# Kernel tuning notes

Hardware: AMD Instinct MI355X
Metric: run time of the kernel (lower is better)

The kernel has to match this reference:

```python
import jax, jax.numpy as jnp
import numpy as np

EPS = 1e-5

def _layernorm(h):
    # parameter-free LayerNorm over last dim (elementwise_affine=False)
    mu = jnp.mean(h, axis=-1, keepdims=True)
    var = jnp.mean(jnp.square(h - mu), axis=-1, keepdims=True)
    return (h - mu) / jnp.sqrt(var + EPS)

def setup_inputs() -> dict:
    key = jax.random.key(0)
    k1, k2, k3, k4 = jax.random.split(key, 4)
    B, D, F_, I = 16, 37, 4096, 64
    x = jax.random.normal(k1, (B, D, F_), dtype=jnp.float32)
    s = 1.0 / np.sqrt(D)  # ~ torch Linear default init scale
    Wq = jax.random.normal(k2, (D, I), dtype=jnp.float32) * s
    Wk = jax.random.normal(k3, (D, I), dtype=jnp.float32) * s
    Wv = jax.random.normal(k4, (D, I), dtype=jnp.float32) * s
    return {"x": x, "Wq": Wq, "Wk": Wk, "Wv": Wv}

def reference(x, Wq, Wk, Wv):
    # x: [B, depth, featuresize] -> entities [B, F, depth]
    xb = jnp.transpose(x, (0, 2, 1))
    q = _layernorm(jnp.einsum('bfd,di->bfi', xb, Wq))
    k = _layernorm(jnp.einsum('bfd,di->bfi', xb, Wk))
    v = _layernorm(jnp.einsum('bfd,di->bfi', xb, Wv))
    d = q.shape[-1]
    att = jnp.einsum('bqi,bki->bqk', q, k) / jnp.sqrt(jnp.float32(d))
    # faithful to torch: softmax over dim=1 (the query axis), not the key axis
    weights = jax.nn.softmax(att, axis=-2)
    return jnp.einsum('bqk,bki->bqi', weights, v)
```

## Files before the change

### kernel.cpp

```cpp
#include <hip/hip_runtime.h>
#include <math.h>

#define B_  16
#define D_  37
#define F_  4096
#define I_  64
#define EPS 1e-5f
#define QSCALE 0.18033688011112042f
#define NQS 2

typedef unsigned short u16;
typedef __bf16 bf16x8 __attribute__((ext_vector_type(8)));
typedef __bf16 bf16x2v __attribute__((ext_vector_type(2)));
typedef float  f32x16 __attribute__((ext_vector_type(16)));
typedef float  f32x2v __attribute__((ext_vector_type(2)));
typedef unsigned int u32x4 __attribute__((ext_vector_type(4)));
typedef int i32x2 __attribute__((ext_vector_type(2)));

#define ZERO16 {0,0,0,0, 0,0,0,0, 0,0,0,0, 0,0,0,0}
#define MFMA32(a, b, c) __builtin_amdgcn_mfma_f32_32x32x16_bf16((a), (b), (c), 0, 0, 0)

#if __has_builtin(__builtin_amdgcn_exp2f)
#define EX2(x) __builtin_amdgcn_exp2f(x)
#else
#define EX2(x) exp2f(x)
#endif
#if __has_builtin(__builtin_amdgcn_rcpf)
#define RCP(x) __builtin_amdgcn_rcpf(x)
#else
#define RCP(x) (1.f / (x))
#endif

__device__ __forceinline__ u16 f2b(float f) {
  unsigned u = __builtin_bit_cast(unsigned, f);
  return (u16)((u + 0x7fffu + ((u >> 16) & 1u)) >> 16);
}
__device__ __forceinline__ float b2f(u16 h) {
  return __builtin_bit_cast(float, (unsigned)h << 16);
}
__device__ __forceinline__ unsigned pk2(float lo, float hi) {
  f32x2v f = {lo, hi};
  bf16x2v h = __builtin_convertvector(f, bf16x2v);
  return __builtin_bit_cast(unsigned, h);
}

__device__ __forceinline__ void plswap(unsigned& a, unsigned& b) {
#if __has_builtin(__builtin_amdgcn_permlane32_swap)
  i32x2 r = __builtin_amdgcn_permlane32_swap((int)a, (int)b, false, false);
  a = (unsigned)r[0];
  b = (unsigned)r[1];
#else
  const int lh = (int)((threadIdx.x & 63) >> 5);
  unsigned pa = (unsigned)__shfl_xor((int)a, 32, 64);
  unsigned pb = (unsigned)__shfl_xor((int)b, 32, 64);
  unsigned na = lh ? pb : a;
  unsigned nb = lh ? b : pa;
  a = na;
  b = nb;
#endif
}

__device__ __forceinline__ void build_af(const f32x16& s, bf16x8& f0, bf16x8& f1) {
  float e[16];
#pragma unroll
  for (int r = 0; r < 16; ++r) e[r] = EX2(s[r]);
  unsigned a = pk2(e[0], e[1]),   bq = pk2(e[2], e[3]);
  unsigned c = pk2(e[4], e[5]),   d  = pk2(e[6], e[7]);
  plswap(a, c);
  plswap(bq, d);
  u32x4 v0 = {a, bq, c, d};
  f0 = __builtin_bit_cast(bf16x8, v0);
  unsigned ee = pk2(e[8], e[9]),  ff = pk2(e[10], e[11]);
  unsigned g  = pk2(e[12], e[13]), h = pk2(e[14], e[15]);
  plswap(ee, g);
  plswap(ff, h);
  u32x4 v1 = {ee, ff, g, h};
  f1 = __builtin_bit_cast(bf16x8, v1);
}

__device__ __forceinline__ bf16x8 ldfrag(const u16* base, int row, int kb) {
  return *(const bf16x8*)(base + (row << 6) + ((kb ^ (row & 7)) << 3));
}
__device__ __forceinline__ void stage16(u16* dst, const u16* src, int c, int spitch) {
  const int r = c >> 3, cb = c & 7;
  const int4 v = *(const int4*)(src + (size_t)r * spitch + (cb << 3));
  *(int4*)(dst + (r << 6) + ((cb ^ (r & 7)) << 3)) = v;
}
__device__ __forceinline__ int soff_l(int c) {
  const int r = c >> 3, cb = c & 7;
  return (r << 6) + ((cb ^ (r & 7)) << 3);
}
__device__ __forceinline__ int soff_g(int c, int spitch) {
  return (c >> 3) * spitch + ((c & 7) << 3);
}

__device__ __forceinline__ int swz512(int wg) {
  return (wg & 7) * 64 + (wg >> 3);
}

__global__ __launch_bounds__(256) void qkv_ln_k(
    const float* __restrict__ x,
    const float* __restrict__ Wq, const float* __restrict__ Wk,
    const float* __restrict__ Wv,
    u16* __restrict__ qn, u16* __restrict__ kn, u16* __restrict__ vt) {
  __shared__ float sW[3 * D_ * I_];
  __shared__ float xs[D_ * 64];
  __shared__ __align__(16) u16 vtile[64 * 72];

  const int t = threadIdx.x;
  const int b = blockIdx.y;
  const int f0 = blockIdx.x * 64;

  for (int i = t; i < D_ * I_; i += 256) {
    sW[i]               = Wq[i];
    sW[D_ * I_ + i]     = Wk[i];
    sW[2 * D_ * I_ + i] = Wv[i];
  }
  const float* xb = x + (size_t)b * D_ * F_ + f0;
  for (int i = t; i < D_ * 64; i += 256)
    xs[i] = xb[(size_t)(i >> 6) * F_ + (i & 63)];
  __syncthreads();

  const int lane = t & 63, w = t >> 6;

  for (int it = 0; it < 16; ++it) {
    const int fl = w * 16 + it;
    float hq = 0.f, hk = 0.f, hv = 0.f;
#pragma unroll
    for (int d = 0; d < D_; ++d) {
      const float xv = xs[d * 64 + fl];
      hq = fmaf(xv, sW[d * 64 + lane], hq);
      hk = fmaf(xv, sW[D_ * I_ + d * 64 + lane], hk);
      hv = fmaf(xv, sW[2 * D_ * I_ + d * 64 + lane], hv);
    }
    auto lnorm = [&](float a) -> float {
      float s = a;
#pragma unroll
      for (int o = 32; o > 0; o >>= 1) s += __shfl_xor(s, o, 64);
      const float mu = s * (1.f / 64.f);
      const float d0 = a - mu;
      float v = d0 * d0;
#pragma unroll
      for (int o = 32; o > 0; o >>= 1) v += __shfl_xor(v, o, 64);
      return d0 * rsqrtf(v * (1.f / 64.f) + EPS);
    };
    const size_t fo = ((size_t)b * F_ + f0 + fl) * I_ + lane;
    qn[fo] = f2b(lnorm(hq) * QSCALE);
    kn[fo] = f2b(lnorm(hk));
    vtile[lane * 72 + fl] = f2b(lnorm(hv));
  }
  __syncthreads();
  for (int p = 0; p < 2; ++p) {
    const int c = p * 256 + t;
    const int r = c >> 3, off = (c & 7) * 8;
    const int4 v = *(const int4*)&vtile[r * 72 + off];
    *(int4*)(vt + ((size_t)b * I_ + r) * F_ + f0 + off) = v;
  }
}

__global__ __launch_bounds__(256, 2) void attn_stats_k(
    const u16* __restrict__ qn, const u16* __restrict__ kn,
    float* __restrict__ zp) {
  __shared__ __align__(16) u16 sm[16384];

  const int t = threadIdx.x, lane = t & 63, w = t >> 6;
  const int l31 = lane & 31, lh = lane >> 5;
  const int lg = swz512((int)blockIdx.x);
  const int k0 = (lg & 15) * 256, b = (lg >> 4) & 15, qh = lg >> 8;

  const u16* kb = kn + ((size_t)b * F_ + k0) * I_;
#pragma unroll
  for (int p = 0; p < 8; ++p) stage16(sm, kb, p * 256 + t, 64);
  __syncthreads();
  bf16x8 kf[2][4];
#pragma unroll
  for (int kb2 = 0; kb2 < 2; ++kb2)
#pragma unroll
    for (int ic = 0; ic < 4; ++ic)
      kf[kb2][ic] = ldfrag(sm + (w * 64 + kb2 * 32) * 64, l31, ic * 2 + lh);
  __syncthreads();

  int qoff_l[2], qoff_g[2];
#pragma unroll
  for (int p = 0; p < 2; ++p) {
    const int c = p * 256 + t;
    qoff_l[p] = soff_l(c);
    qoff_g[p] = soff_g(c, 64);
  }

  const u16* qsrc = qn + ((size_t)b * F_ + qh * (F_ / NQS)) * I_;
#pragma unroll
  for (int p = 0; p < 2; ++p)
    *(int4*)(sm + qoff_l[p]) = *(const int4*)(qsrc + qoff_g[p]);
  qsrc += 64 * I_;

  float Zc[2][2] = {{0.f, 0.f}, {0.f, 0.f}};
  const int NC = F_ / NQS / 64;

  for (int c = 0; c < NC; ++c) {
    const int cur = (c & 1) * 4096;
    int4 qr0, qr1;
    const bool pf = (c + 1 < NC);
    if (pf) {
      qr0 = *(const int4*)(qsrc + qoff_g[0]);
      qr1 = *(const int4*)(qsrc + qoff_g[1]);
      qsrc += 64 * I_;
    }
    __syncthreads();

    f32x16 a00 = ZERO16, a01 = ZERO16, a10 = ZERO16, a11 = ZERO16;
    __builtin_amdgcn_s_setprio(1);
#pragma unroll
    for (int ic = 0; ic < 4; ++ic) {
      const bf16x8 q0f = ldfrag(sm + cur, l31, ic * 2 + lh);
      const bf16x8 q1f = ldfrag(sm + cur + 32 * 64, l31, ic * 2 + lh);
      a00 = MFMA32(q0f, kf[0][ic], a00);
      a01 = MFMA32(q0f, kf[1][ic], a01);
      a10 = MFMA32(q1f, kf[0][ic], a10);
      a11 = MFMA32(q1f, kf[1][ic], a11);
    }
    __builtin_amdgcn_s_setprio(0);
#pragma unroll
    for (int r = 0; r < 16; ++r) {
      Zc[0][0] += EX2(a00[r]);
      Zc[0][1] += EX2(a01[r]);
      Zc[1][0] += EX2(a10[r]);
      Zc[1][1] += EX2(a11[r]);
    }

    if (pf) {
      const int nxt = cur ^ 4096;
      *(int4*)(sm + nxt + qoff_l[0]) = qr0;
      *(int4*)(sm + nxt + qoff_l[1]) = qr1;
    }
  }

#pragma unroll
  for (int kb2 = 0; kb2 < 2; ++kb2) {
    float Zt = Zc[0][kb2] + Zc[1][kb2];
    Zt += __shfl_xor(Zt, 32, 64);
    if (lane < 32)
      zp[((size_t)qh * B_ + b) * F_ + k0 + w * 64 + kb2 * 32 + lane] = Zt;
  }
}

__global__ __launch_bounds__(256) void vscale_k(u16* __restrict__ vt,
                                                const float* __restrict__ zp) {
  const int b = blockIdx.y;
  const int off = (blockIdx.x * 256 + (int)threadIdx.x) * 8;
  const int k = off & (F_ - 1);
  const size_t BF = (size_t)B_ * F_;
  u16* p = vt + (size_t)b * I_ * F_ + off;
  const float* z = zp + (size_t)b * F_ + k;
  int4 raw = *(const int4*)p;
  u16 es[8], os[8];
  *(int4*)es = raw;
#pragma unroll
  for (int j = 0; j < 8; ++j) {
    const float v = b2f(es[j]);
    float zs = 0.f;
#pragma unroll
    for (int qh = 0; qh < NQS; ++qh) zs += z[qh * BF + j];
    os[j] = f2b(v * RCP(zs));
  }
  *(int4*)p = *(int4*)os;
}

__global__ __launch_bounds__(256, 2) void attn_out_k(
    const u16* __restrict__ qn, const u16* __restrict__ kn,
    const u16* __restrict__ vt, float* __restrict__ out,
    u16* __restrict__ pout) {
  __shared__ __align__(16) u16 sm[16384];

  const int t = threadIdx.x, lane = t & 63, w = t >> 6;
  const int l31 = lane & 31, lh = lane >> 5;
  const int lg = swz512((int)blockIdx.x);
  const int q0 = (lg & 15) * 256, b = (lg >> 4) & 15, ks = lg >> 8;

  const u16* qb = qn + ((size_t)b * F_ + q0) * I_;
#pragma unroll
  for (int p = 0; p < 8; ++p) stage16(sm, qb, p * 256 + t, 64);
  __syncthreads();
  bf16x8 qf[2][4];
#pragma unroll
  for (int qb2 = 0; qb2 < 2; ++qb2)
#pragma unroll
    for (int ic = 0; ic < 4; ++ic)
      qf[qb2][ic] = ldfrag(sm + (w * 64 + qb2 * 32) * 64, l31, ic * 2 + lh);
  __syncthreads();

  int off_l[2], kg[2], vg[2];
#pragma unroll
  for (int p = 0; p < 2; ++p) {
    const int c = p * 256 + t;
    off_l[p] = soff_l(c);
    kg[p] = soff_g(c, 64);
    vg[p] = soff_g(c, F_);
  }

  const u16* ksrc = kn + ((size_t)b * F_ + ks * (F_ / 2)) * I_;
  const u16* vsrc = vt + (size_t)b * I_ * F_ + ks * (F_ / 2);
#pragma unroll
  for (int p = 0; p < 2; ++p) {
    *(int4*)(sm + off_l[p])        = *(const int4*)(ksrc + kg[p]);
    *(int4*)(sm + 8192 + off_l[p]) = *(const int4*)(vsrc + vg[p]);
  }
  ksrc += 64 * I_;
  vsrc += 64;

  f32x16 o00 = ZERO16, o01 = ZERO16, o10 = ZERO16, o11 = ZERO16;
  const int NC = F_ / 2 / 64;

  for (int c = 0; c < NC; ++c) {
    const int cur = (c & 1) * 4096;
    int4 kr0, kr1, vr0, vr1;
    const bool pf = (c + 1 < NC);
    if (pf) {
      kr0 = *(const int4*)(ksrc + kg[0]);
      kr1 = *(const int4*)(ksrc + kg[1]);
      vr0 = *(const int4*)(vsrc + vg[0]);
      vr1 = *(const int4*)(vsrc + vg[1]);
      ksrc += 64 * I_;
      vsrc += 64;
    }
    __syncthreads();

    const u16* Kc = sm + cur;
    f32x16 s00 = ZERO16, s01 = ZERO16, s10 = ZERO16, s11 = ZERO16;
    __builtin_amdgcn_s_setprio(1);
#pragma unroll
    for (int ic = 0; ic < 4; ++ic) {
      const bf16x8 ak0 = ldfrag(Kc, l31, ic * 2 + lh);
      const bf16x8 ak1 = ldfrag(Kc + 32 * 64, l31, ic * 2 + lh);
      s00 = MFMA32(ak0, qf[0][ic], s00);
      s01 = MFMA32(ak0, qf[1][ic], s01);
      s10 = MFMA32(ak1, qf[0][ic], s10);
      s11 = MFMA32(ak1, qf[1][ic], s11);
    }
    __builtin_amdgcn_s_setprio(0);

    bf16x8 af[2][4];
    build_af(s00, af[0][0], af[0][1]);
    build_af(s10, af[0][2], af[0][3]);
    build_af(s01, af[1][0], af[1][1]);
    build_af(s11, af[1][2], af[1][3]);

    const u16* Vc = sm + 8192 + cur;
    __builtin_amdgcn_s_setprio(1);
#pragma unroll
    for (int kb4 = 0; kb4 < 4; ++kb4) {
      const bf16x8 bv0 = ldfrag(Vc, l31, kb4 * 2 + lh);
      const bf16x8 bv1 = ldfrag(Vc + 32 * 64, l31, kb4 * 2 + lh);
      o00 = MFMA32(af[0][kb4], bv0, o00);
      o01 = MFMA32(af[0][kb4], bv1, o01);
      o10 = MFMA32(af[1][kb4], bv0, o10);
      o11 = MFMA32(af[1][kb4], bv1, o11);
    }
    __builtin_amdgcn_s_setprio(0);

    if (pf) {
      const int nxt = cur ^ 4096;
      *(int4*)(sm + nxt + off_l[0])        = kr0;
      *(int4*)(sm + nxt + off_l[1])        = kr1;
      *(int4*)(sm + 8192 + nxt + off_l[0]) = vr0;
      *(int4*)(sm + 8192 + nxt + off_l[1]) = vr1;
    }
  }

  if (ks == 0) {
    float* ob = out + ((size_t)b * F_ + q0 + w * 64) * I_;
#pragma unroll
    for (int r = 0; r < 16; ++r) {
      const int qr = (r & 3) + 8 * (r >> 2) + 4 * lh;
      ob[(size_t)qr * I_ + l31]              = o00[r];
      ob[(size_t)qr * I_ + 32 + l31]         = o01[r];
      ob[(size_t)(32 + qr) * I_ + l31]       = o10[r];
      ob[(size_t)(32 + qr) * I_ + 32 + l31]  = o11[r];
    }
  } else {
    u16* pb = pout + ((size_t)b * F_ + q0 + w * 64) * I_;
#pragma unroll
    for (int r = 0; r < 16; ++r) {
      const int qr = (r & 3) + 8 * (r >> 2) + 4 * lh;
      pb[(size_t)qr * I_ + l31]              = f2b(o00[r]);
      pb[(size_t)qr * I_ + 32 + l31]         = f2b(o01[r]);
      pb[(size_t)(32 + qr) * I_ + l31]       = f2b(o10[r]);
      pb[(size_t)(32 + qr) * I_ + 32 + l31]  = f2b(o11[r]);
    }
  }
}

__global__ __launch_bounds__(256) void reduce_k(float* __restrict__ out,
                                                const u16* __restrict__ pout) {
  const size_t i = ((size_t)blockIdx.x * 256 + threadIdx.x) * 8;
  float4 a0 = *(const float4*)(out + i);
  float4 a1 = *(const float4*)(out + i + 4);
  int4 praw = *(const int4*)(pout + i);
  u16 es[8];
  *(int4*)es = praw;
  a0.x += b2f(es[0]); a0.y += b2f(es[1]); a0.z += b2f(es[2]); a0.w += b2f(es[3]);
  a1.x += b2f(es[4]); a1.y += b2f(es[5]); a1.z += b2f(es[6]); a1.w += b2f(es[7]);
  *(float4*)(out + i)     = a0;
  *(float4*)(out + i + 4) = a1;
}

extern "C" void kernel_launch(void* const* d_in, const int* in_sizes, int n_in,
                              void* d_out, int out_size, void* d_ws,
                              size_t ws_size, hipStream_t stream) {
  const float* x  = (const float*)d_in[0];
  const float* Wq = (const float*)d_in[1];
  const float* Wk = (const float*)d_in[2];
  const float* Wv = (const float*)d_in[3];
  float* out = (float*)d_out;

  const size_t NBF = (size_t)B_ * F_ * I_;
  u16* qn   = (u16*)d_ws;
  u16* kn   = qn + NBF;
  u16* vt   = kn + NBF;
  float* zp = (float*)(vt + NBF);
  u16* pout = (u16*)(zp + (size_t)NQS * B_ * F_);

  qkv_ln_k<<<dim3(F_ / 64, B_), 256, 0, stream>>>(x, Wq, Wk, Wv, qn, kn, vt);
  attn_stats_k<<<dim3(512), 256, 0, stream>>>(qn, kn, zp);
  vscale_k<<<dim3(I_ * F_ / 2048, B_), 256, 0, stream>>>(vt, zp);
  attn_out_k<<<dim3(512), 256, 0, stream>>>(qn, kn, vt, out, pout);
  reduce_k<<<dim3((int)(NBF / 2048)), 256, 0, stream>>>(out, pout);
}
```

Baseline: 234.6 us.

## Split attention into four query/key slices with fp32 partials and half-tile scoring

Doubles the grid of both attention kernels by splitting the stats pass into four query slices and the output pass into four key slices. Partial outputs are now written as fp32 instead of bf16, and reduce_k sums three partial planes. The inner loop computes scores one 32-row key half at a time to cut live registers, and launch bounds rise to three blocks per SM. This buys more parallelism and occupancy at the cost of more partial-output traffic and a heavier reduction.

Result: slower. 314.2 us (+33.9%).

```diff
diff --git a/kernel.cpp b/kernel.cpp
--- a/kernel.cpp
+++ b/kernel.cpp
@@ -7,7 +7,8 @@
 #define I_  64
 #define EPS 1e-5f
 #define QSCALE 0.18033688011112042f
-#define NQS 2
+#define NQS 4
+#define NKS 4
 
 typedef unsigned short u16;
 typedef __bf16 bf16x8 __attribute__((ext_vector_type(8)));
@@ -94,8 +95,8 @@
   return (c >> 3) * spitch + ((c & 7) << 3);
 }
 
-__device__ __forceinline__ int swz512(int wg) {
-  return (wg & 7) * 64 + (wg >> 3);
+__device__ __forceinline__ int swz1024(int wg) {
+  return (wg & 7) * 128 + (wg >> 3);
 }
 
 __global__ __launch_bounds__(256) void qkv_ln_k(
@@ -158,14 +159,14 @@
   }
 }
 
-__global__ __launch_bounds__(256, 2) void attn_stats_k(
+__global__ __launch_bounds__(256, 3) void attn_stats_k(
     const u16* __restrict__ qn, const u16* __restrict__ kn,
     float* __restrict__ zp) {
   __shared__ __align__(16) u16 sm[16384];
 
   const int t = threadIdx.x, lane = t & 63, w = t >> 6;
   const int l31 = lane & 31, lh = lane >> 5;
-  const int lg = swz512((int)blockIdx.x);
+  const int lg = swz1024((int)blockIdx.x);
   const int k0 = (lg & 15) * 256, b = (lg >> 4) & 15, qh = lg >> 8;
 
   const u16* kb = kn + ((size_t)b * F_ + k0) * I_;
@@ -266,15 +267,15 @@
   *(int4*)p = *(int4*)os;
 }
 
-__global__ __launch_bounds__(256, 2) void attn_out_k(
+__global__ __launch_bounds__(256, 3) void attn_out_k(
     const u16* __restrict__ qn, const u16* __restrict__ kn,
     const u16* __restrict__ vt, float* __restrict__ out,
-    u16* __restrict__ pout) {
+    float* __restrict__ pp) {
   __shared__ __align__(16) u16 sm[16384];
 
   const int t = threadIdx.x, lane = t & 63, w = t >> 6;
   const int l31 = lane & 31, lh = lane >> 5;
-  const int lg = swz512((int)blockIdx.x);
+  const int lg = swz1024((int)blockIdx.x);
   const int q0 = (lg & 15) * 256, b = (lg >> 4) & 15, ks = lg >> 8;
 
   const u16* qb = qn + ((size_t)b * F_ + q0) * I_;
@@ -298,8 +299,8 @@
     vg[p] = soff_g(c, F_);
   }
 
-  const u16* ksrc = kn + ((size_t)b * F_ + ks * (F_ / 2)) * I_;
-  const u16* vsrc = vt + (size_t)b * I_ * F_ + ks * (F_ / 2);
+  const u16* ksrc = kn + ((size_t)b * F_ + ks * (F_ / NKS)) * I_;
+  const u16* vsrc = vt + (size_t)b * I_ * F_ + ks * (F_ / NKS);
 #pragma unroll
   for (int p = 0; p < 2; ++p) {
     *(int4*)(sm + off_l[p])        = *(const int4*)(ksrc + kg[p]);
@@ -309,7 +310,7 @@
   vsrc += 64;
 
   f32x16 o00 = ZERO16, o01 = ZERO16, o10 = ZERO16, o11 = ZERO16;
-  const int NC = F_ / 2 / 64;
+  const int NC = F_ / NKS / 64;
 
   for (int c = 0; c < NC; ++c) {
     const int cur = (c & 1) * 4096;
@@ -326,37 +327,59 @@
     __syncthreads();
 
     const u16* Kc = sm + cur;
-    f32x16 s00 = ZERO16, s01 = ZERO16, s10 = ZERO16, s11 = ZERO16;
-    __builtin_amdgcn_s_setprio(1);
-#pragma unroll
-    for (int ic = 0; ic < 4; ++ic) {
-      const bf16x8 ak0 = ldfrag(Kc, l31, ic * 2 + lh);
-      const bf16x8 ak1 = ldfrag(Kc + 32 * 64, l31, ic * 2 + lh);
-      s00 = MFMA32(ak0, qf[0][ic], s00);
-      s01 = MFMA32(ak0, qf[1][ic], s01);
-      s10 = MFMA32(ak1, qf[0][ic], s10);
-      s11 = MFMA32(ak1, qf[1][ic], s11);
-    }
-    __builtin_amdgcn_s_setprio(0);
-
-    bf16x8 af[2][4];
-    build_af(s00, af[0][0], af[0][1]);
-    build_af(s10, af[0][2], af[0][3]);
-    build_af(s01, af[1][0], af[1][1]);
-    build_af(s11, af[1][2], af[1][3]);
-
     const u16* Vc = sm + 8192 + cur;
-    __builtin_amdgcn_s_setprio(1);
-#pragma unroll
-    for (int kb4 = 0; kb4 < 4; ++kb4) {
-      const bf16x8 bv0 = ldfrag(Vc, l31, kb4 * 2 + lh);
-      const bf16x8 bv1 = ldfrag(Vc + 32 * 64, l31, kb4 * 2 + lh);
-      o00 = MFMA32(af[0][kb4], bv0, o00);
-      o01 = MFMA32(af[0][kb4], bv1, o01);
-      o10 = MFMA32(af[1][kb4], bv0, o10);
-      o11 = MFMA32(af[1][kb4], bv1, o11);
-    }
-    __builtin_amdgcn_s_setprio(0);
+
+    {
+      f32x16 s0 = ZERO16, s1 = ZERO16;
+      __builtin_amdgcn_s_setprio(1);
+#pragma unroll
+      for (int ic = 0; ic < 4; ++ic) {
+        const bf16x8 ak = ldfrag(Kc, l31, ic * 2 + lh);
+        s0 = MFMA32(ak, qf[0][ic], s0);
+        s1 = MFMA32(ak, qf[1][ic], s1);
+      }
+      __builtin_amdgcn_s_setprio(0);
+      bf16x8 af[2][2];
+      build_af(s0, af[0][0], af[0][1]);
+      build_af(s1, af[1][0], af[1][1]);
+      __builtin_amdgcn_s_setprio(1);
+#pragma unroll
+      for (int kb4 = 0; kb4 < 2; ++kb4) {
+        const bf16x8 bv0 = ldfrag(Vc, l31, kb4 * 2 + lh);
+        const bf16x8 bv1 = ldfrag(Vc + 32 * 64, l31, kb4 * 2 + lh);
+        o00 = MFMA32(af[0][kb4], bv0, o00);
+        o01 = MFMA32(af[0][kb4], bv1, o01);
+        o10 = MFMA32(af[1][kb4], bv0, o10);
+        o11 = MFMA32(af[1][kb4], bv1, o11);
+      }
+      __builtin_amdgcn_s_setprio(0);
+    }
+
+    {
+      f32x16 s0 = ZERO16, s1 = ZERO16;
+      __builtin_amdgcn_s_setprio(1);
+#pragma unroll
+      for (int ic = 0; ic < 4; ++ic) {
+        const bf16x8 ak = ldfrag(Kc + 32 * 64, l31, ic * 2 + lh);
+        s0 = MFMA32(ak, qf[0][ic], s0);
+        s1 = MFMA32(ak, qf[1][ic], s1);
+      }
+      __builtin_amdgcn_s_setprio(0);
+      bf16x8 af[2][2];
+      build_af(s0, af[0][0], af[0][1]);
+      build_af(s1, af[1][0], af[1][1]);
+      __builtin_amdgcn_s_setprio(1);
+#pragma unroll
+      for (int kb4 = 2; kb4 < 4; ++kb4) {
+        const bf16x8 bv0 = ldfrag(Vc, l31, kb4 * 2 + lh);
+        const bf16x8 bv1 = ldfrag(Vc + 32 * 64, l31, kb4 * 2 + lh);
+        o00 = MFMA32(af[0][kb4 - 2], bv0, o00);
+        o01 = MFMA32(af[0][kb4 - 2], bv1, o01);
+        o10 = MFMA32(af[1][kb4 - 2], bv0, o10);
+        o11 = MFMA32(af[1][kb4 - 2], bv1, o11);
+      }
+      __builtin_amdgcn_s_setprio(0);
+    }
 
     if (pf) {
       const int nxt = cur ^ 4096;
@@ -367,39 +390,33 @@
     }
   }
 
-  if (ks == 0) {
-    float* ob = out + ((size_t)b * F_ + q0 + w * 64) * I_;
-#pragma unroll
-    for (int r = 0; r < 16; ++r) {
-      const int qr = (r & 3) + 8 * (r >> 2) + 4 * lh;
-      ob[(size_t)qr * I_ + l31]              = o00[r];
-      ob[(size_t)qr * I_ + 32 + l31]         = o01[r];
-      ob[(size_t)(32 + qr) * I_ + l31]       = o10[r];
-      ob[(size_t)(32 + qr) * I_ + 32 + l31]  = o11[r];
-    }
-  } else {
-    u16* pb = pout + ((size_t)b * F_ + q0 + w * 64) * I_;
-#pragma unroll
-    for (int r = 0; r < 16; ++r) {
-      const int qr = (r & 3) + 8 * (r >> 2) + 4 * lh;
-      pb[(size_t)qr * I_ + l31]              = f2b(o00[r]);
-      pb[(size_t)qr * I_ + 32 + l31]         = f2b(o01[r]);
-      pb[(size_t)(32 + qr) * I_ + l31]       = f2b(o10[r]);
-      pb[(size_t)(32 + qr) * I_ + 32 + l31]  = f2b(o11[r]);
-    }
+  float* ob = (ks == 0 ? out
+                       : pp + (size_t)(ks - 1) * ((size_t)B_ * F_ * I_)) +
+              ((size_t)b * F_ + q0 + w * 64) * I_;
+#pragma unroll
+  for (int r = 0; r < 16; ++r) {
+    const int qr = (r & 3) + 8 * (r >> 2) + 4 * lh;
+    ob[(size_t)qr * I_ + l31]              = o00[r];
+    ob[(size_t)qr * I_ + 32 + l31]         = o01[r];
+    ob[(size_t)(32 + qr) * I_ + l31]       = o10[r];
+    ob[(size_t)(32 + qr) * I_ + 32 + l31]  = o11[r];
   }
 }
 
 __global__ __launch_bounds__(256) void reduce_k(float* __restrict__ out,
-                                                const u16* __restrict__ pout) {
+                                                const float* __restrict__ pp) {
+  const size_t NBF = (size_t)B_ * F_ * I_;
   const size_t i = ((size_t)blockIdx.x * 256 + threadIdx.x) * 8;
   float4 a0 = *(const float4*)(out + i);
   float4 a1 = *(const float4*)(out + i + 4);
-  int4 praw = *(const int4*)(pout + i);
-  u16 es[8];
-  *(int4*)es = praw;
-  a0.x += b2f(es[0]); a0.y += b2f(es[1]); a0.z += b2f(es[2]); a0.w += b2f(es[3]);
-  a1.x += b2f(es[4]); a1.y += b2f(es[5]); a1.z += b2f(es[6]); a1.w += b2f(es[7]);
+#pragma unroll
+  for (int pl = 0; pl < NKS - 1; ++pl) {
+    const float* q = pp + (size_t)pl * NBF + i;
+    const float4 b0 = *(const float4*)q;
+    const float4 b1 = *(const float4*)(q + 4);
+    a0.x += b0.x; a0.y += b0.y; a0.z += b0.z; a0.w += b0.w;
+    a1.x += b1.x; a1.y += b1.y; a1.z += b1.z; a1.w += b1.w;
+  }
   *(float4*)(out + i)     = a0;
   *(float4*)(out + i + 4) = a1;
 }
@@ -418,11 +435,11 @@
   u16* kn   = qn + NBF;
   u16* vt   = kn + NBF;
   float* zp = (float*)(vt + NBF);
-  u16* pout = (u16*)(zp + (size_t)NQS * B_ * F_);
+  float* pp = zp + (size_t)NQS * B_ * F_;
 
   qkv_ln_k<<<dim3(F_ / 64, B_), 256, 0, stream>>>(x, Wq, Wk, Wv, qn, kn, vt);
-  attn_stats_k<<<dim3(512), 256, 0, stream>>>(qn, kn, zp);
+  attn_stats_k<<<dim3(1024), 256, 0, stream>>>(qn, kn, zp);
   vscale_k<<<dim3(I_ * F_ / 2048, B_), 256, 0, stream>>>(vt, zp);
-  attn_out_k<<<dim3(512), 256, 0, stream>>>(qn, kn, vt, out, pout);
-  reduce_k<<<dim3((int)(NBF / 2048)), 256, 0, stream>>>(out, pout);
-}
+  attn_out_k<<<dim3(1024), 256, 0, stream>>>(qn, kn, vt, out, pp);
+  reduce_k<<<dim3((int)(NBF / 2048)), 256, 0, stream>>>(out, pp);
+}
```

## Stage two 64-row tiles per barrier and load resident fragments directly from global

Applied to the files above, without the earlier changes.

Both attention kernels now double-buffer 128-row chunks split into two 64-row halves. Each loop iteration needs only one __syncthreads, and the global loads for the second half are issued between the two half computations. The resident K (stats kernel) and Q (output kernel) MFMA fragments are read straight from global memory into registers instead of being staged through shared memory, which drops two barriers and an LDS round trip. The output kernel's shared memory doubles to 64 KB, which may limit occupancy under the two-blocks-per-CU launch bound.

Result: no change. 232.9 us (-0.7%).

```diff
diff --git a/kernel.cpp b/kernel.cpp
--- a/kernel.cpp
+++ b/kernel.cpp
@@ -8,6 +8,7 @@
 #define EPS 1e-5f
 #define QSCALE 0.18033688011112042f
 #define NQS 2
+#define NKS 2
 
 typedef unsigned short u16;
 typedef __bf16 bf16x8 __attribute__((ext_vector_type(8)));
@@ -81,11 +82,6 @@
 __device__ __forceinline__ bf16x8 ldfrag(const u16* base, int row, int kb) {
   return *(const bf16x8*)(base + (row << 6) + ((kb ^ (row & 7)) << 3));
 }
-__device__ __forceinline__ void stage16(u16* dst, const u16* src, int c, int spitch) {
-  const int r = c >> 3, cb = c & 7;
-  const int4 v = *(const int4*)(src + (size_t)r * spitch + (cb << 3));
-  *(int4*)(dst + (r << 6) + ((cb ^ (r & 7)) << 3)) = v;
-}
 __device__ __forceinline__ int soff_l(int c) {
   const int r = c >> 3, cb = c & 7;
   return (r << 6) + ((cb ^ (r & 7)) << 3);
@@ -168,17 +164,13 @@
   const int lg = swz512((int)blockIdx.x);
   const int k0 = (lg & 15) * 256, b = (lg >> 4) & 15, qh = lg >> 8;
 
-  const u16* kb = kn + ((size_t)b * F_ + k0) * I_;
-#pragma unroll
-  for (int p = 0; p < 8; ++p) stage16(sm, kb, p * 256 + t, 64);
-  __syncthreads();
+  const u16* kp = kn + ((size_t)b * F_ + k0 + w * 64 + l31) * I_ + lh * 8;
   bf16x8 kf[2][4];
 #pragma unroll
   for (int kb2 = 0; kb2 < 2; ++kb2)
 #pragma unroll
     for (int ic = 0; ic < 4; ++ic)
-      kf[kb2][ic] = ldfrag(sm + (w * 64 + kb2 * 32) * 64, l31, ic * 2 + lh);
-  __syncthreads();
+      kf[kb2][ic] = *(const bf16x8*)(kp + kb2 * 32 * I_ + ic * 16);
 
   int qoff_l[2], qoff_g[2];
 #pragma unroll
@@ -190,30 +182,22 @@
 
   const u16* qsrc = qn + ((size_t)b * F_ + qh * (F_ / NQS)) * I_;
 #pragma unroll
-  for (int p = 0; p < 2; ++p)
-    *(int4*)(sm + qoff_l[p]) = *(const int4*)(qsrc + qoff_g[p]);
-  qsrc += 64 * I_;
+  for (int s = 0; s < 2; ++s)
+#pragma unroll
+    for (int p = 0; p < 2; ++p)
+      *(int4*)(sm + s * 4096 + qoff_l[p]) =
+          *(const int4*)(qsrc + s * 64 * I_ + qoff_g[p]);
+  qsrc += 128 * I_;
 
   float Zc[2][2] = {{0.f, 0.f}, {0.f, 0.f}};
-  const int NC = F_ / NQS / 64;
-
-  for (int c = 0; c < NC; ++c) {
-    const int cur = (c & 1) * 4096;
-    int4 qr0, qr1;
-    const bool pf = (c + 1 < NC);
-    if (pf) {
-      qr0 = *(const int4*)(qsrc + qoff_g[0]);
-      qr1 = *(const int4*)(qsrc + qoff_g[1]);
-      qsrc += 64 * I_;
-    }
-    __syncthreads();
-
+
+  auto qcompute = [&](const u16* Qc) {
     f32x16 a00 = ZERO16, a01 = ZERO16, a10 = ZERO16, a11 = ZERO16;
     __builtin_amdgcn_s_setprio(1);
 #pragma unroll
     for (int ic = 0; ic < 4; ++ic) {
-      const bf16x8 q0f = ldfrag(sm + cur, l31, ic * 2 + lh);
-      const bf16x8 q1f = ldfrag(sm + cur + 32 * 64, l31, ic * 2 + lh);
+      const bf16x8 q0f = ldfrag(Qc, l31, ic * 2 + lh);
+      const bf16x8 q1f = ldfrag(Qc + 32 * 64, l31, ic * 2 + lh);
       a00 = MFMA32(q0f, kf[0][ic], a00);
       a01 = MFMA32(q0f, kf[1][ic], a01);
       a10 = MFMA32(q1f, kf[0][ic], a10);
@@ -227,11 +211,32 @@
       Zc[1][0] += EX2(a10[r]);
       Zc[1][1] += EX2(a11[r]);
     }
-
-    if (pf) {
-      const int nxt = cur ^ 4096;
+  };
+
+  const int NC = F_ / NQS / 128;
+
+  for (int c = 0; c < NC; ++c) {
+    const int cur = (c & 1) * 8192;
+    const int nxt = cur ^ 8192;
+    const bool pf = (c + 1 < NC);
+    __syncthreads();
+    int4 qr0, qr1;
+    if (pf) {
+      qr0 = *(const int4*)(qsrc + qoff_g[0]);
+      qr1 = *(const int4*)(qsrc + qoff_g[1]);
+    }
+    qcompute(sm + cur);
+    if (pf) {
       *(int4*)(sm + nxt + qoff_l[0]) = qr0;
       *(int4*)(sm + nxt + qoff_l[1]) = qr1;
+      qr0 = *(const int4*)(qsrc + 64 * I_ + qoff_g[0]);
+      qr1 = *(const int4*)(qsrc + 64 * I_ + qoff_g[1]);
+    }
+    qcompute(sm + cur + 4096);
+    if (pf) {
+      *(int4*)(sm + nxt + 4096 + qoff_l[0]) = qr0;
+      *(int4*)(sm + nxt + 4096 + qoff_l[1]) = qr1;
+      qsrc += 128 * I_;
     }
   }
 
@@ -270,24 +275,20 @@
     const u16* __restrict__ qn, const u16* __restrict__ kn,
     const u16* __restrict__ vt, float* __restrict__ out,
     u16* __restrict__ pout) {
-  __shared__ __align__(16) u16 sm[16384];
+  __shared__ __align__(16) u16 sm[32768];
 
   const int t = threadIdx.x, lane = t & 63, w = t >> 6;
   const int l31 = lane & 31, lh = lane >> 5;
   const int lg = swz512((int)blockIdx.x);
   const int q0 = (lg & 15) * 256, b = (lg >> 4) & 15, ks = lg >> 8;
 
-  const u16* qb = qn + ((size_t)b * F_ + q0) * I_;
-#pragma unroll
-  for (int p = 0; p < 8; ++p) stage16(sm, qb, p * 256 + t, 64);
-  __syncthreads();
+  const u16* qp = qn + ((size_t)b * F_ + q0 + w * 64 + l31) * I_ + lh * 8;
   bf16x8 qf[2][4];
 #pragma unroll
   for (int qb2 = 0; qb2 < 2; ++qb2)
 #pragma unroll
     for (int ic = 0; ic < 4; ++ic)
-      qf[qb2][ic] = ldfrag(sm + (w * 64 + qb2 * 32) * 64, l31, ic * 2 + lh);
-  __syncthreads();
+      qf[qb2][ic] = *(const bf16x8*)(qp + qb2 * 32 * I_ + ic * 16);
 
   int off_l[2], kg[2], vg[2];
 #pragma unroll
@@ -298,34 +299,23 @@
     vg[p] = soff_g(c, F_);
   }
 
-  const u16* ksrc = kn + ((size_t)b * F_ + ks * (F_ / 2)) * I_;
-  const u16* vsrc = vt + (size_t)b * I_ * F_ + ks * (F_ / 2);
-#pragma unroll
-  for (int p = 0; p < 2; ++p) {
-    *(int4*)(sm + off_l[p])        = *(const int4*)(ksrc + kg[p]);
-    *(int4*)(sm + 8192 + off_l[p]) = *(const int4*)(vsrc + vg[p]);
-  }
-  ksrc += 64 * I_;
-  vsrc += 64;
+  const u16* ksrc = kn + ((size_t)b * F_ + ks * (F_ / NKS)) * I_;
+  const u16* vsrc = vt + (size_t)b * I_ * F_ + ks * (F_ / NKS);
+#pragma unroll
+  for (int s = 0; s < 2; ++s)
+#pragma unroll
+    for (int p = 0; p < 2; ++p) {
+      *(int4*)(sm + s * 4096 + off_l[p]) =
+          *(const int4*)(ksrc + s * 64 * I_ + kg[p]);
+      *(int4*)(sm + 16384 + s * 4096 + off_l[p]) =
+          *(const int4*)(vsrc + s * 64 + vg[p]);
+    }
+  ksrc += 128 * I_;
+  vsrc += 128;
 
   f32x16 o00 = ZERO16, o01 = ZERO16, o10 = ZERO16, o11 = ZERO16;
-  const int NC = F_ / 2 / 64;
-
-  for (int c = 0; c < NC; ++c) {
-    const int cur = (c & 1) * 4096;
-    int4 kr0, kr1, vr0, vr1;
-    const bool pf = (c + 1 < NC);
-    if (pf) {
-      kr0 = *(const int4*)(ksrc + kg[0]);
-      kr1 = *(const int4*)(ksrc + kg[1]);
-      vr0 = *(const int4*)(vsrc + vg[0]);
-      vr1 = *(const int4*)(vsrc + vg[1]);
-      ksrc += 64 * I_;
-      vsrc += 64;
-    }
-    __syncthreads();
-
-    const u16* Kc = sm + cur;
+
+  auto compute64 = [&](const u16* Kc, const u16* Vc) {
     f32x16 s00 = ZERO16, s01 = ZERO16, s10 = ZERO16, s11 = ZERO16;
     __builtin_amdgcn_s_setprio(1);
 #pragma unroll
@@ -345,7 +335,6 @@
     build_af(s01, af[1][0], af[1][1]);
     build_af(s11, af[1][2], af[1][3]);
 
-    const u16* Vc = sm + 8192 + cur;
     __builtin_amdgcn_s_setprio(1);
 #pragma unroll
     for (int kb4 = 0; kb4 < 4; ++kb4) {
@@ -357,13 +346,41 @@
       o11 = MFMA32(af[1][kb4], bv1, o11);
     }
     __builtin_amdgcn_s_setprio(0);
-
-    if (pf) {
-      const int nxt = cur ^ 4096;
-      *(int4*)(sm + nxt + off_l[0])        = kr0;
-      *(int4*)(sm + nxt + off_l[1])        = kr1;
-      *(int4*)(sm + 8192 + nxt + off_l[0]) = vr0;
-      *(int4*)(sm + 8192 + nxt + off_l[1]) = vr1;
+  };
+
+  const int NC = F_ / NKS / 128;
+
+  for (int c = 0; c < NC; ++c) {
+    const int cur = (c & 1) * 8192;
+    const int nxt = cur ^ 8192;
+    const bool pf = (c + 1 < NC);
+    __syncthreads();
+    int4 kr0, kr1, vr0, vr1;
+    if (pf) {
+      kr0 = *(const int4*)(ksrc + kg[0]);
+      kr1 = *(const int4*)(ksrc + kg[1]);
+      vr0 = *(const int4*)(vsrc + vg[0]);
+      vr1 = *(const int4*)(vsrc + vg[1]);
+    }
+    compute64(sm + cur, sm + 16384 + cur);
+    if (pf) {
+      *(int4*)(sm + nxt + off_l[0])         = kr0;
+      *(int4*)(sm + nxt + off_l[1])         = kr1;
+      *(int4*)(sm + 16384 + nxt + off_l[0]) = vr0;
+      *(int4*)(sm + 16384 + nxt + off_l[1]) = vr1;
+      kr0 = *(const int4*)(ksrc + 64 * I_ + kg[0]);
+      kr1 = *(const int4*)(ksrc + 64 * I_ + kg[1]);
+      vr0 = *(const int4*)(vsrc + 64 + vg[0]);
+      vr1 = *(const int4*)(vsrc + 64 + vg[1]);
+    }
+    compute64(sm + cur + 4096, sm + 16384 + cur + 4096);
+    if (pf) {
+      *(int4*)(sm + nxt + 4096 + off_l[0])         = kr0;
+      *(int4*)(sm + nxt + 4096 + off_l[1])         = kr1;
+      *(int4*)(sm + 16384 + nxt + 4096 + off_l[0]) = vr0;
+      *(int4*)(sm + 16384 + nxt + 4096 + off_l[1]) = vr1;
+      ksrc += 128 * I_;
+      vsrc += 128;
     }
   }
 
```
